# Optimization experiments

Hardware: AMD Instinct MI355X
Metric: run time of the kernel (lower is better)

Reference implementation:

```python
import jax, jax.numpy as jnp
import numpy as np

N = 100_000
E = 1_600_000
IN_F, E_F, OUT_F = 32, 16, 32


def _glorot(key, shape):
    lim = np.sqrt(6.0 / (shape[0] + shape[1])).astype(np.float32)
    return jax.random.uniform(key, shape, jnp.float32, -lim, lim)


def setup_inputs() -> dict:
    key = jax.random.key(0)
    ks = jax.random.split(key, 12)
    return {
        'h_feat': jax.random.normal(ks[0], (N, IN_F), jnp.float32),
        'e_feat': jax.random.normal(ks[1], (N, E_F), jnp.float32),
        'rain0': jax.random.normal(ks[2], (N,), jnp.float32),
        'w_xx': jax.random.uniform(ks[3], (E,), jnp.float32),
        'w_yy': jax.random.uniform(ks[4], (E,), jnp.float32),
        'W_trans': _glorot(ks[5], (E_F + IN_F, OUT_F)),            # transform_h (no bias)
        'W_rin': _glorot(ks[6], (OUT_F + 4 * E_F, 4 * OUT_F)),     # Rainfall_in (no bias)
        'W_rout': _glorot(ks[7], (4 * OUT_F, 1)),                  # Rainfall_out (no bias)
        'src_xx': jax.random.randint(ks[8], (E,), 0, N, jnp.int32),
        'dst_xx': jax.random.randint(ks[9], (E,), 0, N, jnp.int32),
        'src_yy': jax.random.randint(ks[10], (E,), 0, N, jnp.int32),
        'dst_yy': jax.random.randint(ks[11], (E,), 0, N, jnp.int32),
    }


def _segsum(msg, dst):
    return jax.ops.segment_sum(msg, dst, num_segments=N)


def reference(h_feat, e_feat, rain0, w_xx, w_yy, W_trans, W_rin, W_rout,
              src_xx, dst_xx, src_yy, dst_yy):
    # node-wise transform: cat(h, e) -> linear -> activation_edge (relu)
    emh = jax.nn.relu(jnp.concatenate([h_feat, e_feat], axis=1) @ W_trans)  # [N, OUT_F]
    # copy_u + sum over both edge types, then activation (relu)
    h = jax.nn.relu(_segsum(emh[src_xx], dst_xx) + _segsum(emh[src_yy], dst_yy))
    # first-order weighted differences of e_feat, scattered to dst
    grad_x = _segsum(w_xx[:, None] * (e_feat[src_xx] - e_feat[dst_xx]), dst_xx)  # [N, E_F]
    grad_y = _segsum(w_yy[:, None] * (e_feat[src_yy] - e_feat[dst_yy]), dst_yy)
    # second-order weighted differences
    grad_2x = _segsum(w_xx[:, None] * (grad_x[src_xx] - grad_x[dst_xx]), dst_xx)
    grad_2y = _segsum(w_yy[:, None] * (grad_y[src_yy] - grad_y[dst_yy]), dst_yy)
    h_cat = jnp.concatenate([h, grad_x, grad_y, grad_2x, grad_2y], axis=1)  # [N, OUT_F+4*E_F]
    rain_h = jax.nn.relu(h_cat @ W_rin)
    rainfall = rain0[:, None] + rain_h @ W_rout  # error_mode=True
    return rainfall, h
```

## Files before the change

### kernel.cpp

```cpp
#include <hip/hip_runtime.h>
#include <hip/hip_bf16.h>

#define NN 100000
#define EE 1600000
#define SCAN_CHUNK 4096
#define NB ((NN + SCAN_CHUNK - 1) / SCAN_CHUNK)
#define OFFP (NN + 8)
#define NRANGE 4
#define RSZ (NN / NRANGE)
#define C_CH 16
#define CHUNK_E (EE / C_CH)
#define BS 1024
#define NBUK ((NN + BS - 1) / BS)
#define P_CH 128
#define PCHUNK_E (EE / P_CH)
#define AP 104

typedef __attribute__((ext_vector_type(8))) short bf16x8;
typedef __attribute__((ext_vector_type(4))) float f32x4;

__device__ inline unsigned short f2bf(float f) {
    unsigned u = __float_as_uint(f);
    return (unsigned short)((u + 0x7FFFu + ((u >> 16) & 1u)) >> 16);
}
__device__ inline float bf2f(unsigned short u) {
    return __uint_as_float(((unsigned)u) << 16);
}

__global__ __launch_bounds__(1024) void fused_th_k(const float* __restrict__ h_feat,
                                                   const float* __restrict__ e_feat,
                                                   const float* __restrict__ W_trans,
                                                   unsigned short* __restrict__ emh_bf,
                                                   unsigned short* __restrict__ ef_bf,
                                                   const int* __restrict__ dst_a,
                                                   const int* __restrict__ dst_b,
                                                   int* __restrict__ partial, int TB) {
    __shared__ float Wl[48 * 32];
    __shared__ int bins[RSZ];
    if ((int)blockIdx.x < TB) {
        for (int i = threadIdx.x; i < 48 * 32; i += 1024) Wl[i] = W_trans[i];
        __syncthreads();
        int t = blockIdx.x * 1024 + threadIdx.x;
        if (t >= NN * 32) return;
        int n = t >> 5, j = t & 31;
        const float* hrow = h_feat + (size_t)n * 32;
        const float* erow = e_feat + (size_t)n * 16;
        float acc = 0.f;
#pragma unroll 8
        for (int k = 0; k < 32; ++k) acc = fmaf(hrow[k], Wl[k * 32 + j], acc);
#pragma unroll 8
        for (int k = 0; k < 16; ++k) acc = fmaf(erow[k], Wl[(32 + k) * 32 + j], acc);
        emh_bf[t] = f2bf(fmaxf(acc, 0.f));
        if (j < 16) ef_bf[(size_t)n * 16 + j] = f2bf(erow[j]);
    } else {
        for (int i = threadIdx.x; i < RSZ; i += 1024) bins[i] = 0;
        __syncthreads();
        const int idx = (int)blockIdx.x - TB;
        const int q = idx & 7;
        const int t = q >> 2;
        const int p = q & 3;
        const int c = idx >> 3;
        const int* dst = t ? dst_b : dst_a;
        const int lo = p * RSZ;
        const long base = (long)c * CHUNK_E;
        for (int i = threadIdx.x * 4; i < CHUNK_E; i += 4096) {
            int4 d = *reinterpret_cast<const int4*>(dst + base + i);
            int x;
            x = d.x - lo; if ((unsigned)x < RSZ) atomicAdd(&bins[x], 1);
            x = d.y - lo; if ((unsigned)x < RSZ) atomicAdd(&bins[x], 1);
            x = d.z - lo; if ((unsigned)x < RSZ) atomicAdd(&bins[x], 1);
            x = d.w - lo; if ((unsigned)x < RSZ) atomicAdd(&bins[x], 1);
        }
        __syncthreads();
        int* pout = partial + (long)(t * C_CH + c) * NN + lo;
        for (int i = threadIdx.x; i < RSZ; i += 1024) pout[i] = bins[i];
    }
}

__global__ __launch_bounds__(1024) void scanA_k(const int* __restrict__ partial,
                                                int* __restrict__ bsum) {
    __shared__ int wsum[16];
    const int b = blockIdx.x;
    const int t = (b >= NB) ? 1 : 0;
    const int i0 = (b % NB) * SCAN_CHUNK + threadIdx.x * 4;
    int4 s = make_int4(0, 0, 0, 0);
    if (i0 < NN) {
#pragma unroll
        for (int c = 0; c < C_CH; ++c) {
            int4 v = *reinterpret_cast<const int4*>(partial + (long)(t * C_CH + c) * NN + i0);
            s.x += v.x; s.y += v.y; s.z += v.z; s.w += v.w;
        }
    }
    int tot = s.x + s.y + s.z + s.w;
#pragma unroll
    for (int d = 32; d; d >>= 1) tot += __shfl_down(tot, d);
    int lane = threadIdx.x & 63, w = threadIdx.x >> 6;
    if (lane == 0) wsum[w] = tot;
    __syncthreads();
    if (threadIdx.x == 0) {
        int sm = 0;
#pragma unroll
        for (int q = 0; q < 16; ++q) sm += wsum[q];
        bsum[b] = sm;
    }
}

__global__ __launch_bounds__(64) void scanB_k(const int* __restrict__ bsum,
                                              int* __restrict__ bbase,
                                              int* __restrict__ off_a,
                                              int* __restrict__ off_b) {
    int lane = threadIdx.x;
    int v = (lane < 2 * NB) ? bsum[lane] : 0;
    int seg = lane / NB;
    int inc = v;
#pragma unroll
    for (int d = 1; d < 64; d <<= 1) {
        int x = __shfl_up(inc, d);
        if (lane >= d && (lane - d) / NB == seg) inc += x;
    }
    int excl = inc - v;
    if (lane < 2 * NB) bbase[lane] = excl;
    if (lane == NB - 1) off_a[NN] = inc;
    if (lane == 2 * NB - 1) off_b[NN] = inc;
}

__global__ __launch_bounds__(1024) void scanC_k(const int* __restrict__ partial,
                                                int* __restrict__ off_a,
                                                int* __restrict__ off_b,
                                                const int* __restrict__ bbase) {
    __shared__ int wsum[16];
    const int b = blockIdx.x;
    const int t = (b >= NB) ? 1 : 0;
    int* off = t ? off_b : off_a;
    const int base0 = bbase[b];
    const int i0 = (b % NB) * SCAN_CHUNK + threadIdx.x * 4;
    int4 s = make_int4(0, 0, 0, 0);
    if (i0 < NN) {
#pragma unroll
        for (int c = 0; c < C_CH; ++c) {
            int4 v = *reinterpret_cast<const int4*>(partial + (long)(t * C_CH + c) * NN + i0);
            s.x += v.x; s.y += v.y; s.z += v.z; s.w += v.w;
        }
    }
    int s1 = s.x, s2 = s1 + s.y, s3 = s2 + s.z, tot = s3 + s.w;
    int lane = threadIdx.x & 63, w = threadIdx.x >> 6;
    int inc = tot;
#pragma unroll
    for (int d = 1; d < 64; d <<= 1) {
        int x = __shfl_up(inc, d);
        if (lane >= d) inc += x;
    }
    if (lane == 63) wsum[w] = inc;
    int texcl = inc - tot;
    __syncthreads();
    if (threadIdx.x == 0) {
        int r = 0;
#pragma unroll
        for (int q = 0; q < 16; ++q) { int x = wsum[q]; wsum[q] = r; r += x; }
    }
    __syncthreads();
    const int base = base0 + wsum[w] + texcl;
    if (i0 < NN)
        *reinterpret_cast<int4*>(off + i0) = make_int4(base, base + s1, base + s2, base + s3);
}

__global__ __launch_bounds__(256) void count2_k(const int* __restrict__ dst_a,
                                                const int* __restrict__ dst_b,
                                                int* __restrict__ count2) {
    __shared__ int bins[NBUK];
    for (int i = threadIdx.x; i < NBUK; i += 256) bins[i] = 0;
    __syncthreads();
    const int t = blockIdx.x >> 7;
    const int c = blockIdx.x & 127;
    const int* dst = t ? dst_b : dst_a;
    const long base = (long)c * PCHUNK_E;
    for (int i = threadIdx.x * 4; i < PCHUNK_E; i += 1024) {
        int4 d = *reinterpret_cast<const int4*>(dst + base + i);
        atomicAdd(&bins[d.x >> 10], 1);
        atomicAdd(&bins[d.y >> 10], 1);
        atomicAdd(&bins[d.z >> 10], 1);
        atomicAdd(&bins[d.w >> 10], 1);
    }
    __syncthreads();
    int* out = count2 + ((long)t * P_CH + c) * NBUK;
    for (int i = threadIdx.x; i < NBUK; i += 256) out[i] = bins[i];
}

__global__ __launch_bounds__(256) void cur2_k(const int* __restrict__ count2,
                                              const int* __restrict__ off_a,
                                              const int* __restrict__ off_b,
                                              int* __restrict__ cur2) {
    int tid = threadIdx.x;
    if (tid >= 2 * NBUK) return;
    int t = tid / NBUK;
    int b = tid % NBUK;
    const int* off = t ? off_b : off_a;
    int run = off[b * BS];
    for (int c = 0; c < P_CH; ++c) {
        long idx = ((long)t * P_CH + c) * NBUK + b;
        int v = count2[idx];
        cur2[idx] = run;
        run += v;
    }
}

__global__ __launch_bounds__(1024) void part_k(const int* __restrict__ dst_a,
                                               const int* __restrict__ src_a,
                                               const float* __restrict__ w_a,
                                               const int* __restrict__ dst_b,
                                               const int* __restrict__ src_b,
                                               const float* __restrict__ w_b,
                                               const int* __restrict__ cur2,
                                               int2* __restrict__ inter_a,
                                               int2* __restrict__ inter_b) {
    __shared__ int lcur[NBUK];
    const int t = blockIdx.x >> 7;
    const int c = blockIdx.x & 127;
    const int* dst = t ? dst_b : dst_a;
    const int* src = t ? src_b : src_a;
    const float* wv = t ? w_b : w_a;
    int2* inter = t ? inter_b : inter_a;
    {
        const int* cin = cur2 + ((long)t * P_CH + c) * NBUK;
        for (int i = threadIdx.x; i < NBUK; i += 1024) lcur[i] = cin[i];
    }
    __syncthreads();
    const long base = (long)c * PCHUNK_E;
    for (int i = threadIdx.x * 4; i < PCHUNK_E; i += 4096) {
        int4 d = *reinterpret_cast<const int4*>(dst + base + i);
        int4 s = *reinterpret_cast<const int4*>(src + base + i);
        float4 w = *reinterpret_cast<const float4*>(wv + base + i);
        int pos;
        pos = atomicAdd(&lcur[d.x >> 10], 1);
        inter[pos] = make_int2(s.x | ((d.x & 1023) << 20), __float_as_int(w.x));
        pos = atomicAdd(&lcur[d.y >> 10], 1);
        inter[pos] = make_int2(s.y | ((d.y & 1023) << 20), __float_as_int(w.y));
        pos = atomicAdd(&lcur[d.z >> 10], 1);
        inter[pos] = make_int2(s.z | ((d.z & 1023) << 20), __float_as_int(w.z));
        pos = atomicAdd(&lcur[d.w >> 10], 1);
        inter[pos] = make_int2(s.w | ((d.w & 1023) << 20), __float_as_int(w.w));
    }
}

__global__ __launch_bounds__(1024) void scat2_k(const int2* __restrict__ inter_a,
                                                const int2* __restrict__ inter_b,
                                                const int* __restrict__ off_a,
                                                const int* __restrict__ off_b,
                                                int2* __restrict__ csr_a,
                                                int2* __restrict__ csr_b) {
    __shared__ int curs[BS];
    const int t = ((int)blockIdx.x >= NBUK) ? 1 : 0;
    const int b = (int)blockIdx.x - t * NBUK;
    const int2* inter = t ? inter_b : inter_a;
    const int* off = t ? off_b : off_a;
    int2* csr = t ? csr_b : csr_a;
    const int n0 = b * BS;
    const int nend = (n0 + BS < NN) ? n0 + BS : NN;
    for (int i = threadIdx.x; i < nend - n0; i += 1024) curs[i] = off[n0 + i];
    __syncthreads();
    const int lo = off[n0];
    const int hi = off[nend];
    for (int i = lo + threadIdx.x; i < hi; i += 1024) {
        int2 e = inter[i];
        int dloc = (e.x >> 20) & 1023;
        int pos = atomicAdd(&curs[dloc], 1);
        csr[pos] = make_int2(e.x & 0xFFFFF, e.y);
    }
}

__global__ __launch_bounds__(256) void pull1_k(const unsigned short* __restrict__ emh_bf,
                                               const unsigned short* __restrict__ ef_bf,
                                               const float* __restrict__ e_feat,
                                               const int2* __restrict__ csr_a,
                                               const int* __restrict__ off_a,
                                               const int2* __restrict__ csr_b,
                                               const int* __restrict__ off_b,
                                               float* __restrict__ out_h,
                                               float* __restrict__ gx,
                                               float* __restrict__ gy,
                                               unsigned short* __restrict__ gx_bf,
                                               unsigned short* __restrict__ gy_bf) {
    int g = blockIdx.x * 256 + threadIdx.x;
    int n = g >> 5, j = g & 31;
    if (n >= NN) return;
    float acc_h = 0.f;

#pragma unroll
    for (int half = 0; half < 2; ++half) {
        const int2* csr = half ? csr_b : csr_a;
        const int* off = half ? off_b : off_a;
        float* gout = half ? gy : gx;
        unsigned short* gbf = half ? gy_bf : gx_bf;
        float acc_g = 0.f, sumw = 0.f;
        int k = off[n], e2 = off[n + 1];
        for (; k + 3 < e2; k += 4) {
            int2 s0 = csr[k], s1 = csr[k + 1], s2 = csr[k + 2], s3 = csr[k + 3];
            float m0 = bf2f(emh_bf[(size_t)s0.x * 32 + j]);
            float m1 = bf2f(emh_bf[(size_t)s1.x * 32 + j]);
            float m2 = bf2f(emh_bf[(size_t)s2.x * 32 + j]);
            float m3 = bf2f(emh_bf[(size_t)s3.x * 32 + j]);
            acc_h += (m0 + m1) + (m2 + m3);
            if (j < 16) {
                float w0 = __int_as_float(s0.y), w1 = __int_as_float(s1.y);
                float w2 = __int_as_float(s2.y), w3 = __int_as_float(s3.y);
                acc_g = fmaf(w0, bf2f(ef_bf[(size_t)s0.x * 16 + j]), acc_g);
                acc_g = fmaf(w1, bf2f(ef_bf[(size_t)s1.x * 16 + j]), acc_g);
                acc_g = fmaf(w2, bf2f(ef_bf[(size_t)s2.x * 16 + j]), acc_g);
                acc_g = fmaf(w3, bf2f(ef_bf[(size_t)s3.x * 16 + j]), acc_g);
                sumw += (w0 + w1) + (w2 + w3);
            }
        }
        for (; k < e2; ++k) {
            int2 s0 = csr[k];
            acc_h += bf2f(emh_bf[(size_t)s0.x * 32 + j]);
            if (j < 16) {
                float w0 = __int_as_float(s0.y);
                acc_g = fmaf(w0, bf2f(ef_bf[(size_t)s0.x * 16 + j]), acc_g);
                sumw += w0;
            }
        }
        if (j < 16) {
            float val = acc_g - sumw * e_feat[(size_t)n * 16 + j];
            gout[(size_t)n * 16 + j] = val;
            gbf[(size_t)n * 16 + j] = f2bf(val);
        }
    }
    out_h[(size_t)n * 32 + j] = fmaxf(acc_h, 0.f);
}

__global__ __launch_bounds__(256) void pull2_k(const float* __restrict__ gx,
                                               const float* __restrict__ gy,
                                               const unsigned short* __restrict__ gx_bf,
                                               const unsigned short* __restrict__ gy_bf,
                                               const int2* __restrict__ csr_a,
                                               const int* __restrict__ off_a,
                                               const int2* __restrict__ csr_b,
                                               const int* __restrict__ off_b,
                                               float* __restrict__ g2x,
                                               float* __restrict__ g2y) {
    int g = blockIdx.x * 256 + threadIdx.x;
    int n = g >> 4, j = g & 15;
    if (n >= NN) return;

#pragma unroll
    for (int half = 0; half < 2; ++half) {
        const int2* csr = half ? csr_b : csr_a;
        const int* off = half ? off_b : off_a;
        const float* gin = half ? gy : gx;
        const unsigned short* gbf = half ? gy_bf : gx_bf;
        float* g2 = half ? g2y : g2x;
        float acc = 0.f, sumw = 0.f;
        int k = off[n], e2 = off[n + 1];
        for (; k + 3 < e2; k += 4) {
            int2 s0 = csr[k], s1 = csr[k + 1], s2 = csr[k + 2], s3 = csr[k + 3];
            float w0 = __int_as_float(s0.y), w1 = __int_as_float(s1.y);
            float w2 = __int_as_float(s2.y), w3 = __int_as_float(s3.y);
            acc = fmaf(w0, bf2f(gbf[(size_t)s0.x * 16 + j]), acc);
            acc = fmaf(w1, bf2f(gbf[(size_t)s1.x * 16 + j]), acc);
            acc = fmaf(w2, bf2f(gbf[(size_t)s2.x * 16 + j]), acc);
            acc = fmaf(w3, bf2f(gbf[(size_t)s3.x * 16 + j]), acc);
            sumw += (w0 + w1) + (w2 + w3);
        }
        for (; k < e2; ++k) {
            int2 s0 = csr[k];
            float w0 = __int_as_float(s0.y);
            acc = fmaf(w0, bf2f(gbf[(size_t)s0.x * 16 + j]), acc);
            sumw += w0;
        }
        g2[(size_t)n * 16 + j] = acc - sumw * gin[(size_t)n * 16 + j];
    }
}

__global__ __launch_bounds__(256) void final_mfma_k(const float* __restrict__ h,
                                                    const float* __restrict__ gx,
                                                    const float* __restrict__ gy,
                                                    const float* __restrict__ g2x,
                                                    const float* __restrict__ g2y,
                                                    const float* __restrict__ rain0,
                                                    const float* __restrict__ W_rin,
                                                    const float* __restrict__ W_rout,
                                                    float* __restrict__ out_rain) {
    __shared__ __align__(16) unsigned short Wt[128 * AP];
    __shared__ __align__(16) unsigned short At[64 * AP];
    __shared__ float Wo[128];
    const int tid = threadIdx.x;

    for (int i = tid; i < 3072; i += 256) {
        int k = i >> 5;
        int c = (i & 31) * 4;
        float4 wv = *reinterpret_cast<const float4*>(W_rin + k * 128 + c);
        Wt[(c + 0) * AP + k] = f2bf(wv.x);
        Wt[(c + 1) * AP + k] = f2bf(wv.y);
        Wt[(c + 2) * AP + k] = f2bf(wv.z);
        Wt[(c + 3) * AP + k] = f2bf(wv.w);
    }
    if (tid < 128) Wo[tid] = W_rout[tid];

    {
        int n = tid >> 2, q = tid & 3;
        int node = blockIdx.x * 64 + n;
        float f[24];
#define LD4(di, p) { float4 v_ = *reinterpret_cast<const float4*>(p); \
                     f[di] = v_.x; f[di+1] = v_.y; f[di+2] = v_.z; f[di+3] = v_.w; }
        if (node < NN) {
            if (q == 0) {
                LD4(0,  h + (size_t)node * 32 + 0);
                LD4(4,  h + (size_t)node * 32 + 4);
                LD4(8,  h + (size_t)node * 32 + 8);
                LD4(12, h + (size_t)node * 32 + 12);
                LD4(16, h + (size_t)node * 32 + 16);
                LD4(20, h + (size_t)node * 32 + 20);
            } else if (q == 1) {
                LD4(0,  h + (size_t)node * 32 + 24);
                LD4(4,  h + (size_t)node * 32 + 28);
                LD4(8,  gx + (size_t)node * 16 + 0);
                LD4(12, gx + (size_t)node * 16 + 4);
                LD4(16, gx + (size_t)node * 16 + 8);
                LD4(20, gx + (size_t)node * 16 + 12);
            } else if (q == 2) {
                LD4(0,  gy + (size_t)node * 16 + 0);
                LD4(4,  gy + (size_t)node * 16 + 4);
                LD4(8,  gy + (size_t)node * 16 + 8);
                LD4(12, gy + (size_t)node * 16 + 12);
                LD4(16, g2x + (size_t)node * 16 + 0);
                LD4(20, g2x + (size_t)node * 16 + 4);
            } else {
                LD4(0,  g2x + (size_t)node * 16 + 8);
                LD4(4,  g2x + (size_t)node * 16 + 12);
                LD4(8,  g2y + (size_t)node * 16 + 0);
                LD4(12, g2y + (size_t)node * 16 + 4);
                LD4(16, g2y + (size_t)node * 16 + 8);
                LD4(20, g2y + (size_t)node * 16 + 12);
            }
        } else {
#pragma unroll
            for (int i = 0; i < 24; ++i) f[i] = 0.f;
        }
#undef LD4
        unsigned pk[12];
#pragma unroll
        for (int i = 0; i < 12; ++i)
            pk[i] = (unsigned)f2bf(f[2 * i]) | ((unsigned)f2bf(f[2 * i + 1]) << 16);
        char* dp = (char*)At + n * (AP * 2) + q * 48;
        *reinterpret_cast<uint4*>(dp + 0)  = make_uint4(pk[0], pk[1], pk[2], pk[3]);
        *reinterpret_cast<uint4*>(dp + 16) = make_uint4(pk[4], pk[5], pk[6], pk[7]);
        *reinterpret_cast<uint4*>(dp + 32) = make_uint4(pk[8], pk[9], pk[10], pk[11]);
    }
    __syncthreads();

    const int w = tid >> 6;
    const int l = tid & 63;
    const int col = l & 15;
    const int kg = l >> 4;
    const char* Ab = (const char*)At + (w * 16 + col) * (AP * 2) + kg * 16;
    const char* Bb = (const char*)Wt + col * (AP * 2) + kg * 16;

    f32x4 acc[8];
#pragma unroll
    for (int ct = 0; ct < 8; ++ct) acc[ct] = (f32x4){0.f, 0.f, 0.f, 0.f};

#pragma unroll
    for (int ks = 0; ks < 3; ++ks) {
        bf16x8 af = *reinterpret_cast<const bf16x8*>(Ab + ks * 64);
#pragma unroll
        for (int ct = 0; ct < 8; ++ct) {
            bf16x8 bfr = *reinterpret_cast<const bf16x8*>(Bb + ct * 16 * (AP * 2) + ks * 64);
            acc[ct] = __builtin_amdgcn_mfma_f32_16x16x32_bf16(af, bfr, acc[ct], 0, 0, 0);
        }
    }

    float s0 = 0.f, s1 = 0.f, s2 = 0.f, s3 = 0.f;
#pragma unroll
    for (int ct = 0; ct < 8; ++ct) {
        float wo = Wo[ct * 16 + col];
        s0 = fmaf(fmaxf(acc[ct][0], 0.f), wo, s0);
        s1 = fmaf(fmaxf(acc[ct][1], 0.f), wo, s1);
        s2 = fmaf(fmaxf(acc[ct][2], 0.f), wo, s2);
        s3 = fmaf(fmaxf(acc[ct][3], 0.f), wo, s3);
    }
#pragma unroll
    for (int m = 1; m < 16; m <<= 1) {
        s0 += __shfl_xor(s0, m);
        s1 += __shfl_xor(s1, m);
        s2 += __shfl_xor(s2, m);
        s3 += __shfl_xor(s3, m);
    }
    if (col == 0) {
        int row = blockIdx.x * 64 + w * 16 + kg * 4;
        if (row + 0 < NN) out_rain[row + 0] = rain0[row + 0] + s0;
        if (row + 1 < NN) out_rain[row + 1] = rain0[row + 1] + s1;
        if (row + 2 < NN) out_rain[row + 2] = rain0[row + 2] + s2;
        if (row + 3 < NN) out_rain[row + 3] = rain0[row + 3] + s3;
    }
}

extern "C" void kernel_launch(void* const* d_in, const int* in_sizes, int n_in,
                              void* d_out, int out_size, void* d_ws, size_t ws_size,
                              hipStream_t stream) {
    const float* h_feat  = (const float*)d_in[0];
    const float* e_feat  = (const float*)d_in[1];
    const float* rain0   = (const float*)d_in[2];
    const float* w_xx    = (const float*)d_in[3];
    const float* w_yy    = (const float*)d_in[4];
    const float* W_trans = (const float*)d_in[5];
    const float* W_rin   = (const float*)d_in[6];
    const float* W_rout  = (const float*)d_in[7];
    const int* src_xx    = (const int*)d_in[8];
    const int* dst_xx    = (const int*)d_in[9];
    const int* src_yy    = (const int*)d_in[10];
    const int* dst_yy    = (const int*)d_in[11];

    unsigned short* emh_bf = (unsigned short*)d_ws;
    unsigned short* ef_bf  = emh_bf + (size_t)NN * 32;
    unsigned short* gx_bf  = ef_bf + (size_t)NN * 16;
    unsigned short* gy_bf  = gx_bf + (size_t)NN * 16;
    float* gx = (float*)(gy_bf + (size_t)NN * 16);
    float* gy = gx + (size_t)NN * 16;
    int2* csr_xx = (int2*)(gy + (size_t)NN * 16);
    int2* csr_yy = csr_xx + EE;
    int* off_xx  = (int*)(csr_yy + EE);
    int* off_yy  = off_xx + OFFP;
    int* partial = off_yy + OFFP;
    int2* inter_xx = (int2*)partial;
    int2* inter_yy = inter_xx + EE;
    float* g2x   = (float*)inter_xx;
    float* g2y   = g2x + (size_t)NN * 16;
    int* tail    = (int*)(inter_yy + EE);
    int* bsum    = tail;
    int* bbase   = bsum + 64;
    int* count2  = bbase + 64;
    int* cur2    = count2 + 2 * P_CH * NBUK;

    float* out_rain = (float*)d_out;
    float* out_h    = out_rain + NN;

    const int TB = (NN * 32 + 1023) / 1024;
    const int HB = 2 * NRANGE * C_CH;
    fused_th_k<<<TB + HB, 1024, 0, stream>>>(h_feat, e_feat, W_trans, emh_bf, ef_bf,
                                             dst_xx, dst_yy, partial, TB);

    scanA_k<<<2 * NB, 1024, 0, stream>>>(partial, bsum);
    scanB_k<<<1, 64, 0, stream>>>(bsum, bbase, off_xx, off_yy);
    scanC_k<<<2 * NB, 1024, 0, stream>>>(partial, off_xx, off_yy, bbase);

    count2_k<<<2 * P_CH, 256, 0, stream>>>(dst_xx, dst_yy, count2);
    cur2_k<<<1, 256, 0, stream>>>(count2, off_xx, off_yy, cur2);

    part_k<<<2 * P_CH, 1024, 0, stream>>>(
        dst_xx, src_xx, w_xx, dst_yy, src_yy, w_yy, cur2, inter_xx, inter_yy);

    scat2_k<<<2 * NBUK, 1024, 0, stream>>>(
        inter_xx, inter_yy, off_xx, off_yy, csr_xx, csr_yy);

    pull1_k<<<(NN * 32 + 255) / 256, 256, 0, stream>>>(
        emh_bf, ef_bf, e_feat, csr_xx, off_xx, csr_yy, off_yy,
        out_h, gx, gy, gx_bf, gy_bf);

    pull2_k<<<(NN * 16 + 255) / 256, 256, 0, stream>>>(
        gx, gy, gx_bf, gy_bf, csr_xx, off_xx, csr_yy, off_yy, g2x, g2y);

    final_mfma_k<<<(NN + 63) / 64, 256, 0, stream>>>(
        out_h, gx, gy, g2x, g2y, rain0, W_rin, W_rout, out_rain);
}
```

Measured before the change: 289.8 us.

## Drop global degree histogram; build CSR offsets in bucket scatter; use fp8 gathers

Removes the full per-node histogram and three scan kernels. Per-bucket totals are now scanned inside a single-block cur2x kernel, and per-node offsets are computed locally in scat2_k with an in-block count and scan before the scatter. Separately, the gathered e_feat and first-order gradient tables are stored as software-encoded fp8 (e4m3-like) instead of bf16, which halves gather bytes but lowers precision and risks tolerance failures.

```diff
diff --git a/kernel.cpp b/kernel.cpp
--- a/kernel.cpp
+++ b/kernel.cpp
@@ -3,13 +3,7 @@
 
 #define NN 100000
 #define EE 1600000
-#define SCAN_CHUNK 4096
-#define NB ((NN + SCAN_CHUNK - 1) / SCAN_CHUNK)
 #define OFFP (NN + 8)
-#define NRANGE 4
-#define RSZ (NN / NRANGE)
-#define C_CH 16
-#define CHUNK_E (EE / C_CH)
 #define BS 1024
 #define NBUK ((NN + BS - 1) / BS)
 #define P_CH 128
@@ -26,142 +20,45 @@
 __device__ inline float bf2f(unsigned short u) {
     return __uint_as_float(((unsigned)u) << 16);
 }
-
-__global__ __launch_bounds__(1024) void fused_th_k(const float* __restrict__ h_feat,
-                                                   const float* __restrict__ e_feat,
-                                                   const float* __restrict__ W_trans,
-                                                   unsigned short* __restrict__ emh_bf,
-                                                   unsigned short* __restrict__ ef_bf,
-                                                   const int* __restrict__ dst_a,
-                                                   const int* __restrict__ dst_b,
-                                                   int* __restrict__ partial, int TB) {
+__device__ inline unsigned char f2fp8(float f) {
+    float a = fabsf(f);
+    if (a < 0.0078125f) return (f < 0.f) ? 0x80 : 0;
+    if (a > 448.f) a = 448.f;
+    unsigned u = __float_as_uint(a);
+    u += 0x0007FFFFu + ((u >> 20) & 1u);
+    int e = ((u >> 23) & 0xFF) - 127;
+    unsigned m = (u >> 20) & 7u;
+    unsigned char b = (unsigned char)(((e + 7) << 3) | m);
+    if (f < 0.f) b |= 0x80;
+    return b;
+}
+__device__ inline float fp82f(unsigned char b) {
+    unsigned e = (b >> 3) & 0xFu;
+    unsigned m = b & 7u;
+    unsigned u = ((unsigned)(b & 0x80u) << 24) | ((e + 120u) << 23) | (m << 20);
+    return (b & 0x7F) ? __uint_as_float(u) : 0.f;
+}
+
+__global__ __launch_bounds__(256) void trans_k(const float* __restrict__ h_feat,
+                                               const float* __restrict__ e_feat,
+                                               const float* __restrict__ W_trans,
+                                               unsigned short* __restrict__ emh_bf,
+                                               unsigned char* __restrict__ ef_f8) {
     __shared__ float Wl[48 * 32];
-    __shared__ int bins[RSZ];
-    if ((int)blockIdx.x < TB) {
-        for (int i = threadIdx.x; i < 48 * 32; i += 1024) Wl[i] = W_trans[i];
-        __syncthreads();
-        int t = blockIdx.x * 1024 + threadIdx.x;
-        if (t >= NN * 32) return;
-        int n = t >> 5, j = t & 31;
-        const float* hrow = h_feat + (size_t)n * 32;
-        const float* erow = e_feat + (size_t)n * 16;
-        float acc = 0.f;
+    for (int i = threadIdx.x; i < 48 * 32; i += 256) Wl[i] = W_trans[i];
+    __syncthreads();
+    int t = blockIdx.x * 256 + threadIdx.x;
+    if (t >= NN * 32) return;
+    int n = t >> 5, j = t & 31;
+    const float* hrow = h_feat + (size_t)n * 32;
+    const float* erow = e_feat + (size_t)n * 16;
+    float acc = 0.f;
 #pragma unroll 8
-        for (int k = 0; k < 32; ++k) acc = fmaf(hrow[k], Wl[k * 32 + j], acc);
+    for (int k = 0; k < 32; ++k) acc = fmaf(hrow[k], Wl[k * 32 + j], acc);
 #pragma unroll 8
-        for (int k = 0; k < 16; ++k) acc = fmaf(erow[k], Wl[(32 + k) * 32 + j], acc);
-        emh_bf[t] = f2bf(fmaxf(acc, 0.f));
-        if (j < 16) ef_bf[(size_t)n * 16 + j] = f2bf(erow[j]);
-    } else {
-        for (int i = threadIdx.x; i < RSZ; i += 1024) bins[i] = 0;
-        __syncthreads();
-        const int idx = (int)blockIdx.x - TB;
-        const int q = idx & 7;
-        const int t = q >> 2;
-        const int p = q & 3;
-        const int c = idx >> 3;
-        const int* dst = t ? dst_b : dst_a;
-        const int lo = p * RSZ;
-        const long base = (long)c * CHUNK_E;
-        for (int i = threadIdx.x * 4; i < CHUNK_E; i += 4096) {
-            int4 d = *reinterpret_cast<const int4*>(dst + base + i);
-            int x;
-            x = d.x - lo; if ((unsigned)x < RSZ) atomicAdd(&bins[x], 1);
-            x = d.y - lo; if ((unsigned)x < RSZ) atomicAdd(&bins[x], 1);
-            x = d.z - lo; if ((unsigned)x < RSZ) atomicAdd(&bins[x], 1);
-            x = d.w - lo; if ((unsigned)x < RSZ) atomicAdd(&bins[x], 1);
-        }
-        __syncthreads();
-        int* pout = partial + (long)(t * C_CH + c) * NN + lo;
-        for (int i = threadIdx.x; i < RSZ; i += 1024) pout[i] = bins[i];
-    }
-}
-
-__global__ __launch_bounds__(1024) void scanA_k(const int* __restrict__ partial,
-                                                int* __restrict__ bsum) {
-    __shared__ int wsum[16];
-    const int b = blockIdx.x;
-    const int t = (b >= NB) ? 1 : 0;
-    const int i0 = (b % NB) * SCAN_CHUNK + threadIdx.x * 4;
-    int4 s = make_int4(0, 0, 0, 0);
-    if (i0 < NN) {
-#pragma unroll
-        for (int c = 0; c < C_CH; ++c) {
-            int4 v = *reinterpret_cast<const int4*>(partial + (long)(t * C_CH + c) * NN + i0);
-            s.x += v.x; s.y += v.y; s.z += v.z; s.w += v.w;
-        }
-    }
-    int tot = s.x + s.y + s.z + s.w;
-#pragma unroll
-    for (int d = 32; d; d >>= 1) tot += __shfl_down(tot, d);
-    int lane = threadIdx.x & 63, w = threadIdx.x >> 6;
-    if (lane == 0) wsum[w] = tot;
-    __syncthreads();
-    if (threadIdx.x == 0) {
-        int sm = 0;
-#pragma unroll
-        for (int q = 0; q < 16; ++q) sm += wsum[q];
-        bsum[b] = sm;
-    }
-}
-
-__global__ __launch_bounds__(64) void scanB_k(const int* __restrict__ bsum,
-                                              int* __restrict__ bbase,
-                                              int* __restrict__ off_a,
-                                              int* __restrict__ off_b) {
-    int lane = threadIdx.x;
-    int v = (lane < 2 * NB) ? bsum[lane] : 0;
-    int seg = lane / NB;
-    int inc = v;
-#pragma unroll
-    for (int d = 1; d < 64; d <<= 1) {
-        int x = __shfl_up(inc, d);
-        if (lane >= d && (lane - d) / NB == seg) inc += x;
-    }
-    int excl = inc - v;
-    if (lane < 2 * NB) bbase[lane] = excl;
-    if (lane == NB - 1) off_a[NN] = inc;
-    if (lane == 2 * NB - 1) off_b[NN] = inc;
-}
-
-__global__ __launch_bounds__(1024) void scanC_k(const int* __restrict__ partial,
-                                                int* __restrict__ off_a,
-                                                int* __restrict__ off_b,
-                                                const int* __restrict__ bbase) {
-    __shared__ int wsum[16];
-    const int b = blockIdx.x;
-    const int t = (b >= NB) ? 1 : 0;
-    int* off = t ? off_b : off_a;
-    const int base0 = bbase[b];
-    const int i0 = (b % NB) * SCAN_CHUNK + threadIdx.x * 4;
-    int4 s = make_int4(0, 0, 0, 0);
-    if (i0 < NN) {
-#pragma unroll
-        for (int c = 0; c < C_CH; ++c) {
-            int4 v = *reinterpret_cast<const int4*>(partial + (long)(t * C_CH + c) * NN + i0);
-            s.x += v.x; s.y += v.y; s.z += v.z; s.w += v.w;
-        }
-    }
-    int s1 = s.x, s2 = s1 + s.y, s3 = s2 + s.z, tot = s3 + s.w;
-    int lane = threadIdx.x & 63, w = threadIdx.x >> 6;
-    int inc = tot;
-#pragma unroll
-    for (int d = 1; d < 64; d <<= 1) {
-        int x = __shfl_up(inc, d);
-        if (lane >= d) inc += x;
-    }
-    if (lane == 63) wsum[w] = inc;
-    int texcl = inc - tot;
-    __syncthreads();
-    if (threadIdx.x == 0) {
-        int r = 0;
-#pragma unroll
-        for (int q = 0; q < 16; ++q) { int x = wsum[q]; wsum[q] = r; r += x; }
-    }
-    __syncthreads();
-    const int base = base0 + wsum[w] + texcl;
-    if (i0 < NN)
-        *reinterpret_cast<int4*>(off + i0) = make_int4(base, base + s1, base + s2, base + s3);
+    for (int k = 0; k < 16; ++k) acc = fmaf(erow[k], Wl[(32 + k) * 32 + j], acc);
+    emh_bf[t] = f2bf(fmaxf(acc, 0.f));
+    if (j < 16) ef_f8[(size_t)n * 16 + j] = f2fp8(erow[j]);
 }
 
 __global__ __launch_bounds__(256) void count2_k(const int* __restrict__ dst_a,
@@ -186,21 +83,43 @@
     for (int i = threadIdx.x; i < NBUK; i += 256) out[i] = bins[i];
 }
 
-__global__ __launch_bounds__(256) void cur2_k(const int* __restrict__ count2,
-                                              const int* __restrict__ off_a,
-                                              const int* __restrict__ off_b,
-                                              int* __restrict__ cur2) {
-    int tid = threadIdx.x;
-    if (tid >= 2 * NBUK) return;
-    int t = tid / NBUK;
-    int b = tid % NBUK;
-    const int* off = t ? off_b : off_a;
-    int run = off[b * BS];
-    for (int c = 0; c < P_CH; ++c) {
-        long idx = ((long)t * P_CH + c) * NBUK + b;
-        int v = count2[idx];
-        cur2[idx] = run;
-        run += v;
+__global__ __launch_bounds__(1024) void cur2x_k(const int* __restrict__ count2,
+                                                int* __restrict__ cur2,
+                                                int* __restrict__ bbase_g) {
+    __shared__ int tot[2 * NBUK];
+    __shared__ int bb[2 * NBUK];
+    const int tid = threadIdx.x;
+    for (int i = tid; i < 2 * NBUK; i += 1024) tot[i] = 0;
+    __syncthreads();
+    for (int idx = tid; idx < 2 * P_CH * NBUK; idx += 1024) {
+        int tb = idx / (P_CH * NBUK);
+        int b = idx % NBUK;
+        atomicAdd(&tot[tb * NBUK + b], count2[idx]);
+    }
+    __syncthreads();
+    if (tid < 2) {
+        int r = 0;
+        for (int b = 0; b < NBUK; ++b) { int x = tot[tid * NBUK + b]; bb[tid * NBUK + b] = r; r += x; }
+    }
+    __syncthreads();
+    for (int i = tid; i < 2 * NBUK; i += 1024) bbase_g[i] = bb[i];
+    const int lane = tid & 63, wid = tid >> 6;
+    for (int u = wid; u < 2 * NBUK; u += 16) {
+        int t = u / NBUK, b = u % NBUK;
+        int base = bb[u];
+        int c0 = lane * 2;
+        long i0 = ((long)t * P_CH + c0) * NBUK + b;
+        long i1 = ((long)t * P_CH + c0 + 1) * NBUK + b;
+        int v0 = count2[i0], v1 = count2[i1];
+        int ps = v0 + v1, inc = ps;
+#pragma unroll
+        for (int d = 1; d < 64; d <<= 1) {
+            int x = __shfl_up(inc, d);
+            if (lane >= d) inc += x;
+        }
+        int excl = inc - ps;
+        cur2[i0] = base + excl;
+        cur2[i1] = base + excl + v0;
     }
 }
 
@@ -244,32 +163,61 @@
 
 __global__ __launch_bounds__(1024) void scat2_k(const int2* __restrict__ inter_a,
                                                 const int2* __restrict__ inter_b,
-                                                const int* __restrict__ off_a,
-                                                const int* __restrict__ off_b,
+                                                const int* __restrict__ bbase_g,
+                                                int* __restrict__ off_a,
+                                                int* __restrict__ off_b,
                                                 int2* __restrict__ csr_a,
                                                 int2* __restrict__ csr_b) {
-    __shared__ int curs[BS];
+    __shared__ int cnt[BS];
+    __shared__ int wsum[16];
+    const int tid = threadIdx.x;
     const int t = ((int)blockIdx.x >= NBUK) ? 1 : 0;
     const int b = (int)blockIdx.x - t * NBUK;
     const int2* inter = t ? inter_b : inter_a;
-    const int* off = t ? off_b : off_a;
+    int* off = t ? off_b : off_a;
     int2* csr = t ? csr_b : csr_a;
     const int n0 = b * BS;
-    const int nend = (n0 + BS < NN) ? n0 + BS : NN;
-    for (int i = threadIdx.x; i < nend - n0; i += 1024) curs[i] = off[n0 + i];
-    __syncthreads();
-    const int lo = off[n0];
-    const int hi = off[nend];
-    for (int i = lo + threadIdx.x; i < hi; i += 1024) {
+    const int nn = ((n0 + BS < NN) ? BS : NN - n0);
+    const int blo = bbase_g[t * NBUK + b];
+    const int bhi = (b < NBUK - 1) ? bbase_g[t * NBUK + b + 1] : EE;
+    cnt[tid] = 0;
+    __syncthreads();
+    for (int i = blo + tid; i < bhi; i += 1024) {
+        int dloc = (inter[i].x >> 20) & 1023;
+        atomicAdd(&cnt[dloc], 1);
+    }
+    __syncthreads();
+    int v = cnt[tid];
+    int lane = tid & 63, wid = tid >> 6;
+    int inc = v;
+#pragma unroll
+    for (int d = 1; d < 64; d <<= 1) {
+        int x = __shfl_up(inc, d);
+        if (lane >= d) inc += x;
+    }
+    if (lane == 63) wsum[wid] = inc;
+    __syncthreads();
+    if (tid == 0) {
+        int r = 0;
+#pragma unroll
+        for (int q = 0; q < 16; ++q) { int x = wsum[q]; wsum[q] = r; r += x; }
+    }
+    __syncthreads();
+    int excl = blo + wsum[wid] + inc - v;
+    if (tid < nn) off[n0 + tid] = excl;
+    if (b == NBUK - 1 && tid == 0) off[NN] = EE;
+    cnt[tid] = excl;
+    __syncthreads();
+    for (int i = blo + tid; i < bhi; i += 1024) {
         int2 e = inter[i];
         int dloc = (e.x >> 20) & 1023;
-        int pos = atomicAdd(&curs[dloc], 1);
+        int pos = atomicAdd(&cnt[dloc], 1);
         csr[pos] = make_int2(e.x & 0xFFFFF, e.y);
     }
 }
 
 __global__ __launch_bounds__(256) void pull1_k(const unsigned short* __restrict__ emh_bf,
-                                               const unsigned short* __restrict__ ef_bf,
+                                               const unsigned char* __restrict__ ef_f8,
                                                const float* __restrict__ e_feat,
                                                const int2* __restrict__ csr_a,
                                                const int* __restrict__ off_a,
@@ -278,8 +226,8 @@
                                                float* __restrict__ out_h,
                                                float* __restrict__ gx,
                                                float* __restrict__ gy,
-                                               unsigned short* __restrict__ gx_bf,
-                                               unsigned short* __restrict__ gy_bf) {
+                                               unsigned char* __restrict__ gx_f8,
+                                               unsigned char* __restrict__ gy_f8) {
     int g = blockIdx.x * 256 + threadIdx.x;
     int n = g >> 5, j = g & 31;
     if (n >= NN) return;
@@ -290,7 +238,7 @@
         const int2* csr = half ? csr_b : csr_a;
         const int* off = half ? off_b : off_a;
         float* gout = half ? gy : gx;
-        unsigned short* gbf = half ? gy_bf : gx_bf;
+        unsigned char* gf8 = half ? gy_f8 : gx_f8;
         float acc_g = 0.f, sumw = 0.f;
         int k = off[n], e2 = off[n + 1];
         for (; k + 3 < e2; k += 4) {
@@ -303,10 +251,10 @@
             if (j < 16) {
                 float w0 = __int_as_float(s0.y), w1 = __int_as_float(s1.y);
                 float w2 = __int_as_float(s2.y), w3 = __int_as_float(s3.y);
-                acc_g = fmaf(w0, bf2f(ef_bf[(size_t)s0.x * 16 + j]), acc_g);
-                acc_g = fmaf(w1, bf2f(ef_bf[(size_t)s1.x * 16 + j]), acc_g);
-                acc_g = fmaf(w2, bf2f(ef_bf[(size_t)s2.x * 16 + j]), acc_g);
-                acc_g = fmaf(w3, bf2f(ef_bf[(size_t)s3.x * 16 + j]), acc_g);
+                acc_g = fmaf(w0, fp82f(ef_f8[(size_t)s0.x * 16 + j]), acc_g);
+                acc_g = fmaf(w1, fp82f(ef_f8[(size_t)s1.x * 16 + j]), acc_g);
+                acc_g = fmaf(w2, fp82f(ef_f8[(size_t)s2.x * 16 + j]), acc_g);
+                acc_g = fmaf(w3, fp82f(ef_f8[(size_t)s3.x * 16 + j]), acc_g);
                 sumw += (w0 + w1) + (w2 + w3);
             }
         }
@@ -315,14 +263,14 @@
             acc_h += bf2f(emh_bf[(size_t)s0.x * 32 + j]);
             if (j < 16) {
                 float w0 = __int_as_float(s0.y);
-                acc_g = fmaf(w0, bf2f(ef_bf[(size_t)s0.x * 16 + j]), acc_g);
+                acc_g = fmaf(w0, fp82f(ef_f8[(size_t)s0.x * 16 + j]), acc_g);
                 sumw += w0;
             }
         }
         if (j < 16) {
             float val = acc_g - sumw * e_feat[(size_t)n * 16 + j];
             gout[(size_t)n * 16 + j] = val;
-            gbf[(size_t)n * 16 + j] = f2bf(val);
+            gf8[(size_t)n * 16 + j] = f2fp8(val);
         }
     }
     out_h[(size_t)n * 32 + j] = fmaxf(acc_h, 0.f);
@@ -330,8 +278,8 @@
 
 __global__ __launch_bounds__(256) void pull2_k(const float* __restrict__ gx,
                                                const float* __restrict__ gy,
-                                               const unsigned short* __restrict__ gx_bf,
-                                               const unsigned short* __restrict__ gy_bf,
+                                               const unsigned char* __restrict__ gx_f8,
+                                               const unsigned char* __restrict__ gy_f8,
                                                const int2* __restrict__ csr_a,
                                                const int* __restrict__ off_a,
                                                const int2* __restrict__ csr_b,
@@ -347,7 +295,7 @@
         const int2* csr = half ? csr_b : csr_a;
         const int* off = half ? off_b : off_a;
         const float* gin = half ? gy : gx;
-        const unsigned short* gbf = half ? gy_bf : gx_bf;
+        const unsigned char* gf8 = half ? gy_f8 : gx_f8;
         float* g2 = half ? g2y : g2x;
         float acc = 0.f, sumw = 0.f;
         int k = off[n], e2 = off[n + 1];
@@ -355,16 +303,16 @@
             int2 s0 = csr[k], s1 = csr[k + 1], s2 = csr[k + 2], s3 = csr[k + 3];
             float w0 = __int_as_float(s0.y), w1 = __int_as_float(s1.y);
             float w2 = __int_as_float(s2.y), w3 = __int_as_float(s3.y);
-            acc = fmaf(w0, bf2f(gbf[(size_t)s0.x * 16 + j]), acc);
-            acc = fmaf(w1, bf2f(gbf[(size_t)s1.x * 16 + j]), acc);
-            acc = fmaf(w2, bf2f(gbf[(size_t)s2.x * 16 + j]), acc);
-            acc = fmaf(w3, bf2f(gbf[(size_t)s3.x * 16 + j]), acc);
+            acc = fmaf(w0, fp82f(gf8[(size_t)s0.x * 16 + j]), acc);
+            acc = fmaf(w1, fp82f(gf8[(size_t)s1.x * 16 + j]), acc);
+            acc = fmaf(w2, fp82f(gf8[(size_t)s2.x * 16 + j]), acc);
+            acc = fmaf(w3, fp82f(gf8[(size_t)s3.x * 16 + j]), acc);
             sumw += (w0 + w1) + (w2 + w3);
         }
         for (; k < e2; ++k) {
             int2 s0 = csr[k];
             float w0 = __int_as_float(s0.y);
-            acc = fmaf(w0, bf2f(gbf[(size_t)s0.x * 16 + j]), acc);
+            acc = fmaf(w0, fp82f(gf8[(size_t)s0.x * 16 + j]), acc);
             sumw += w0;
         }
         g2[(size_t)n * 16 + j] = acc - sumw * gin[(size_t)n * 16 + j];
@@ -511,53 +459,44 @@
     const int* dst_yy    = (const int*)d_in[11];
 
     unsigned short* emh_bf = (unsigned short*)d_ws;
-    unsigned short* ef_bf  = emh_bf + (size_t)NN * 32;
-    unsigned short* gx_bf  = ef_bf + (size_t)NN * 16;
-    unsigned short* gy_bf  = gx_bf + (size_t)NN * 16;
-    float* gx = (float*)(gy_bf + (size_t)NN * 16);
+    unsigned char* ef_f8 = (unsigned char*)(emh_bf + (size_t)NN * 32);
+    unsigned char* gx_f8 = ef_f8 + (size_t)NN * 16;
+    unsigned char* gy_f8 = gx_f8 + (size_t)NN * 16;
+    float* gx = (float*)(gy_f8 + (size_t)NN * 16);
     float* gy = gx + (size_t)NN * 16;
     int2* csr_xx = (int2*)(gy + (size_t)NN * 16);
     int2* csr_yy = csr_xx + EE;
     int* off_xx  = (int*)(csr_yy + EE);
     int* off_yy  = off_xx + OFFP;
-    int* partial = off_yy + OFFP;
-    int2* inter_xx = (int2*)partial;
+    int2* inter_xx = (int2*)(off_yy + OFFP);
     int2* inter_yy = inter_xx + EE;
     float* g2x   = (float*)inter_xx;
     float* g2y   = g2x + (size_t)NN * 16;
-    int* tail    = (int*)(inter_yy + EE);
-    int* bsum    = tail;
-    int* bbase   = bsum + 64;
-    int* count2  = bbase + 64;
+    int* count2  = (int*)(inter_yy + EE);
     int* cur2    = count2 + 2 * P_CH * NBUK;
+    int* bbase_g = cur2 + 2 * P_CH * NBUK;
 
     float* out_rain = (float*)d_out;
     float* out_h    = out_rain + NN;
 
-    const int TB = (NN * 32 + 1023) / 1024;
-    const int HB = 2 * NRANGE * C_CH;
-    fused_th_k<<<TB + HB, 1024, 0, stream>>>(h_feat, e_feat, W_trans, emh_bf, ef_bf,
-                                             dst_xx, dst_yy, partial, TB);
-
-    scanA_k<<<2 * NB, 1024, 0, stream>>>(partial, bsum);
-    scanB_k<<<1, 64, 0, stream>>>(bsum, bbase, off_xx, off_yy);
-    scanC_k<<<2 * NB, 1024, 0, stream>>>(partial, off_xx, off_yy, bbase);
+    trans_k<<<(NN * 32 + 255) / 256, 256, 0, stream>>>(h_feat, e_feat, W_trans,
+                                                       emh_bf, ef_f8);
 
     count2_k<<<2 * P_CH, 256, 0, stream>>>(dst_xx, dst_yy, count2);
-    cur2_k<<<1, 256, 0, stream>>>(count2, off_xx, off_yy, cur2);
+    cur2x_k<<<1, 1024, 0, stream>>>(count2, cur2, bbase_g);
 
     part_k<<<2 * P_CH, 1024, 0, stream>>>(
         dst_xx, src_xx, w_xx, dst_yy, src_yy, w_yy, cur2, inter_xx, inter_yy);
 
     scat2_k<<<2 * NBUK, 1024, 0, stream>>>(
-        inter_xx, inter_yy, off_xx, off_yy, csr_xx, csr_yy);
+        inter_xx, inter_yy, bbase_g, off_xx, off_yy, csr_xx, csr_yy);
 
     pull1_k<<<(NN * 32 + 255) / 256, 256, 0, stream>>>(
-        emh_bf, ef_bf, e_feat, csr_xx, off_xx, csr_yy, off_yy,
-        out_h, gx, gy, gx_bf, gy_bf);
+        emh_bf, ef_f8, e_feat, csr_xx, off_xx, csr_yy, off_yy,
+        out_h, gx, gy, gx_f8, gy_f8);
 
     pull2_k<<<(NN * 16 + 255) / 256, 256, 0, stream>>>(
-        gx, gy, gx_bf, gy_bf, csr_xx, off_xx, csr_yy, off_yy, g2x, g2y);
+        gx, gy, gx_f8, gy_f8, csr_xx, off_xx, csr_yy, off_yy, g2x, g2y);
 
     final_mfma_k<<<(NN + 63) / 64, 256, 0, stream>>>(
         out_h, gx, gy, g2x, g2y, rain0, W_rin, W_rout, out_rain);
```

Measured after the change: 372.0 us. 1.28x slower.
